# Kernel tuning notes

Measured on AMD Instinct MI355X. Metric: run time of the kernel, lower is better.

The kernel has to match this reference:

```python
import jax, jax.numpy as jnp
import numpy as np

E = 131072   # total messages
N = 8192     # dim_size (num nodes)
D = 256      # input_dim == hidden_dim (forced by h + m add)


def setup_inputs() -> dict:
    key = jax.random.key(0)
    k1, k2, k3, k4, k5 = jax.random.split(key, 5)
    msg = jax.random.normal(k1, (E, D), dtype=jnp.float32)
    index = jax.random.randint(k2, (E,), 0, N)
    t = jax.random.uniform(k3, (E,), dtype=jnp.float32)
    # torch.nn.Linear(D, D) params (kaiming-uniform-ish scale)
    W = jax.random.normal(k4, (D, D), dtype=jnp.float32) / np.sqrt(D)
    b = (jax.random.normal(k5, (D,), dtype=jnp.float32) * 0.01)
    return {"msg": msg, "index": index, "t": t, "dim_size": N, "W": W, "b": b}


def reference(msg, index, t, dim_size, W, b):
    # Original: for each node, sort its messages by t, then run the linear
    # recurrence h <- W @ (m + h) + b starting from h = 0; nodes with no
    # messages keep h = 0. Vectorized: one global stable sort by (index, t),
    # then a single segmented lax.scan with reset at segment boundaries.
    num_msgs, d = msg.shape
    order = jnp.lexsort((t, index))          # primary key: index, secondary: t
    m_sorted = msg[order]                     # [E, d]
    seg = index[order]                        # [E]

    def step(carry, inp):
        h, prev = carry
        m, s = inp
        h_in = jnp.where(s == prev, h, jnp.zeros_like(h))  # reset at new segment
        h_new = (m + h_in) @ W.T + b
        return (h_new, s), h_new

    init = (jnp.zeros((d,), msg.dtype), jnp.asarray(-1, seg.dtype))
    _, ys = jax.lax.scan(step, init, (m_sorted, seg))      # ys: [E, d]

    # final hidden per node = h at the last message of its segment
    pos = jnp.arange(num_msgs)
    last = jax.ops.segment_max(pos, seg, num_segments=dim_size)
    counts = jax.ops.segment_sum(jnp.ones((num_msgs,), jnp.int32), seg,
                                 num_segments=dim_size)
    gathered = ys[jnp.clip(last, 0, num_msgs - 1)]          # [N, d]
    hidden = jnp.where((counts > 0)[:, None], gathered, jnp.zeros_like(gathered))
    return hidden
```

## Files before the change

### kernel.cpp

```cpp
#include <hip/hip_runtime.h>
#include <hip/hip_bf16.h>

#define E_MSGS 131072
#define N_NODES 8192
#define D_DIM 256
#define XA_STRIDE 264

typedef __bf16 bf16x8 __attribute__((ext_vector_type(8)));
typedef float f32x4 __attribute__((ext_vector_type(4)));

#define BAR() asm volatile("s_waitcnt lgkmcnt(0)\n\ts_barrier" ::: "memory")


__global__ void k_count(const int* __restrict__ index, int* __restrict__ counts) {
    int e = blockIdx.x * blockDim.x + threadIdx.x;
    if (e < E_MSGS) atomicAdd(&counts[index[e]], 1);
}

__global__ void k_scan(const int* __restrict__ counts, int* __restrict__ offsets,
                       int* __restrict__ cursors) {
    __shared__ int wsum[16], wpre[16];
    int tid = threadIdx.x, lane = tid & 63, wave = tid >> 6;
    int base = tid * 8;
    int4 c0 = *(const int4*)(counts + base);
    int4 c1 = *(const int4*)(counts + base + 4);
    int v[8] = {c0.x, c0.y, c0.z, c0.w, c1.x, c1.y, c1.z, c1.w};
    int loc[8], sum = 0;
#pragma unroll
    for (int i = 0; i < 8; i++) { loc[i] = sum; sum += v[i]; }
    int incl = sum;
#pragma unroll
    for (int d = 1; d < 64; d <<= 1) {
        int u = __shfl_up(incl, d);
        if (lane >= d) incl += u;
    }
    if (lane == 63) wsum[wave] = incl;
    __syncthreads();
    if (tid < 16) {
        int w = wsum[tid], p = w;
#pragma unroll
        for (int d = 1; d < 16; d <<= 1) {
            int u = __shfl_up(p, d);
            if (tid >= d) p += u;
        }
        wpre[tid] = p - w;
    }
    __syncthreads();
    int ebase = wpre[wave] + incl - sum;
#pragma unroll
    for (int i = 0; i < 8; i++) offsets[base + i] = ebase + loc[i];
    int4 z = {0, 0, 0, 0};
    *(int4*)(cursors + base) = z;
    *(int4*)(cursors + base + 4) = z;
    if (tid == 0) offsets[N_NODES] = E_MSGS;
}

__global__ void k_scatter(const int* __restrict__ index, const int* __restrict__ offsets,
                          int* __restrict__ cursors, int* __restrict__ bucket) {
    int e = blockIdx.x * blockDim.x + threadIdx.x;
    if (e < E_MSGS) {
        int n = index[e];
        int p = offsets[n] + atomicAdd(&cursors[n], 1);
        bucket[p] = e;
    }
}


#define GRU_STEP(SS, CUR, NXT)                                                 \
    {                                                                          \
        _Pragma("unroll") for (int r = 0; r < 4; r++) {                        \
            const float* mrow = msg + (long)sidR[r] * D_DIM;                   \
            _Pragma("unroll") for (int t4 = 0; t4 < 4; t4++)                   \
                NXT[r][t4] = mrow[64 * wave + 16 * t4 + l];                     \
        }                                                                      \
        {                                                                      \
            int row = (SS) + 3 < 64 ? (SS) + 3 : 63;                           \
            int4 sr = *(const int4*)&sid[row][4 * q];                          \
            sidR[0] = sr.x; sidR[1] = sr.y; sidR[2] = sr.z; sidR[3] = sr.w;    \
        }                                                                      \
        const __bf16* buf = xA[(SS) & 1];                                      \
        f32x4 acc[4];                                                          \
        _Pragma("unroll") for (int t4 = 0; t4 < 4; t4++)                       \
            acc[t4] = (f32x4){0.f, 0.f, 0.f, 0.f};                             \
        _Pragma("unroll") for (int c = 0; c < 8; c++) {                        \
            bf16x8 a = *(const bf16x8*)(buf + l * XA_STRIDE + 32 * c + 8 * q); \
            _Pragma("unroll") for (int t4 = 0; t4 < 4; t4++)                   \
                acc[t4] = __builtin_amdgcn_mfma_f32_16x16x32_bf16(             \
                    a, wf[c][t4], acc[t4], 0, 0, 0);                           \
        }                                                                      \
        __bf16* nbuf = xA[((SS) + 1) & 1];                                     \
        _Pragma("unroll") for (int t4 = 0; t4 < 4; t4++) {                     \
            _Pragma("unroll") for (int r = 0; r < 4; r++) {                    \
                float hn = acc[t4][r] + bias[t4];                              \
                bool valid = (SS) < cnt4[r];                                   \
                h[t4][r] = valid ? hn : h[t4][r];                              \
                nbuf[(4 * q + r) * XA_STRIDE + 64 * wave + 16 * t4 + l] =      \
                    (__bf16)(h[t4][r] + CUR[r][t4]);                           \
            }                                                                  \
        }                                                                      \
        BAR();                                                                 \
    }

__launch_bounds__(256, 2)
__global__ void k_gru(const float* __restrict__ msg, const float* __restrict__ t,
                      const int* __restrict__ bucket, const float* __restrict__ W,
                      const float* __restrict__ b, const int* __restrict__ offsets,
                      float* __restrict__ out) {
    __shared__ __bf16 xA[2][16 * XA_STRIDE];
    __shared__ int sid[64][16];

    int tid = threadIdx.x;
    int wave = tid >> 6, lane = tid & 63, q = lane >> 4, l = lane & 15;
    int node0 = blockIdx.x * 16;

    bf16x8 wf[8][4];
#pragma unroll
    for (int t4 = 0; t4 < 4; t4++) {
        const float* wr = W + (64 * wave + 16 * t4 + l) * D_DIM;
#pragma unroll
        for (int c = 0; c < 8; c++) {
            int k0 = 32 * c + 8 * q;
            float4 w0 = *(const float4*)(wr + k0);
            float4 w1 = *(const float4*)(wr + k0 + 4);
            bf16x8 f;
            f[0] = (__bf16)w0.x; f[1] = (__bf16)w0.y; f[2] = (__bf16)w0.z; f[3] = (__bf16)w0.w;
            f[4] = (__bf16)w1.x; f[5] = (__bf16)w1.y; f[6] = (__bf16)w1.z; f[7] = (__bf16)w1.w;
            wf[c][t4] = f;
        }
    }
    float bias[4];
#pragma unroll
    for (int t4 = 0; t4 < 4; t4++) bias[t4] = b[64 * wave + 16 * t4 + l];

    int off4[4], cnt4[4];
#pragma unroll
    for (int r = 0; r < 4; r++) {
        off4[r] = offsets[node0 + 4 * q + r];
        cnt4[r] = offsets[node0 + 4 * q + r + 1] - off4[r];
    }
    int mc = max(max(cnt4[0], cnt4[1]), max(cnt4[2], cnt4[3]));
    mc = max(mc, __shfl_xor(mc, 16));
    mc = max(mc, __shfl_xor(mc, 32));
    int S = mc;

    for (int i = 0; i < 4; i++) {
        int j = 4 * wave + i;
        int beg = offsets[node0 + j];
        int cnt = min(offsets[node0 + j + 1] - beg, 64);
        sid[lane][j] = 0;
        int e = 0; float tv = 0.f;
        if (lane < cnt) { e = bucket[beg + lane]; tv = t[e]; }
        int rank = 0;
        for (int j2 = 0; j2 < cnt; j2++) {
            float tj = __shfl(tv, j2);
            int ej = __shfl(e, j2);
            rank += (tj < tv) || (tj == tv && ej < e);
        }
        if (lane < cnt) sid[rank][j] = e;
    }
    BAR();

    float h[4][4];
#pragma unroll
    for (int t4 = 0; t4 < 4; t4++)
#pragma unroll
        for (int r = 0; r < 4; r++) h[t4][r] = 0.f;

    float mvA[4][4], mvB[4][4];
    int sidR[4];
    int4 sr0 = *(const int4*)&sid[0][4 * q];
    int4 sr1 = *(const int4*)&sid[1][4 * q];
    int4 sr2 = *(const int4*)&sid[2][4 * q];
    int s0[4] = {sr0.x, sr0.y, sr0.z, sr0.w};
    int s1[4] = {sr1.x, sr1.y, sr1.z, sr1.w};
    sidR[0] = sr2.x; sidR[1] = sr2.y; sidR[2] = sr2.z; sidR[3] = sr2.w;
#pragma unroll
    for (int r = 0; r < 4; r++) {
        const float* m0 = msg + (long)s0[r] * D_DIM;
        const float* m1 = msg + (long)s1[r] * D_DIM;
#pragma unroll
        for (int t4 = 0; t4 < 4; t4++) {
            int col = 64 * wave + 16 * t4 + l;
            xA[0][(4 * q + r) * XA_STRIDE + col] = (__bf16)m0[col];
            mvA[r][t4] = m1[col];
        }
    }
    BAR();

    int s = 0;
    while (s < S) {
        GRU_STEP(s, mvA, mvB); s++;
        if (s >= S) break;
        GRU_STEP(s, mvB, mvA); s++;
    }

#pragma unroll
    for (int t4 = 0; t4 < 4; t4++)
#pragma unroll
        for (int r = 0; r < 4; r++)
            out[(long)(node0 + 4 * q + r) * D_DIM + 64 * wave + 16 * t4 + l] = h[t4][r];
}


extern "C" void kernel_launch(void* const* d_in, const int* in_sizes, int n_in,
                              void* d_out, int out_size, void* d_ws, size_t ws_size,
                              hipStream_t stream) {
    const float* msg   = (const float*)d_in[0];
    const int*   index = (const int*)d_in[1];
    const float* t     = (const float*)d_in[2];
    const float* W     = (const float*)d_in[4];
    const float* b     = (const float*)d_in[5];
    float* out = (float*)d_out;

    int* ws = (int*)d_ws;
    int* counts  = ws;
    int* cursors = ws + 8192;
    int* offsets = ws + 16384;
    int* bucket  = ws + 24584;

    hipMemsetAsync(counts, 0, 8192 * sizeof(int), stream);

    k_count<<<E_MSGS / 256, 256, 0, stream>>>(index, counts);
    k_scan<<<1, 1024, 0, stream>>>(counts, offsets, cursors);
    k_scatter<<<E_MSGS / 256, 256, 0, stream>>>(index, offsets, cursors, bucket);
    k_gru<<<N_NODES / 16, 256, 0, stream>>>(msg, t, bucket, W, b, offsets, out);
}
```

Measured before the change: 266.3 us.

## Bucket messages into fixed 64-slot padded arrays and sort nodes by count

Replaces the count/scan/scatter CSR build with a single atomic scatter into fixed 64-slot per-node buckets, which drops one kernel and the prefix scan. A new single-block kernel counting-sorts nodes by message count, descending. Each GRU block then processes 16 nodes of similar length, so fewer recurrence steps are wasted on padding. It also raises wave priority around the MFMA loop. The cost is a hard cap of 64 messages per node, which silently drops the rest, and scattered output writes.

```diff
diff --git a/kernel.cpp b/kernel.cpp
--- a/kernel.cpp
+++ b/kernel.cpp
@@ -12,56 +12,37 @@
 #define BAR() asm volatile("s_waitcnt lgkmcnt(0)\n\ts_barrier" ::: "memory")
 
 
-__global__ void k_count(const int* __restrict__ index, int* __restrict__ counts) {
+__global__ void k_scatter(const int* __restrict__ index, int* __restrict__ cursors,
+                          int* __restrict__ pad) {
     int e = blockIdx.x * blockDim.x + threadIdx.x;
-    if (e < E_MSGS) atomicAdd(&counts[index[e]], 1);
-}
-
-__global__ void k_scan(const int* __restrict__ counts, int* __restrict__ offsets,
-                       int* __restrict__ cursors) {
-    __shared__ int wsum[16], wpre[16];
-    int tid = threadIdx.x, lane = tid & 63, wave = tid >> 6;
-    int base = tid * 8;
-    int4 c0 = *(const int4*)(counts + base);
-    int4 c1 = *(const int4*)(counts + base + 4);
-    int v[8] = {c0.x, c0.y, c0.z, c0.w, c1.x, c1.y, c1.z, c1.w};
-    int loc[8], sum = 0;
-#pragma unroll
-    for (int i = 0; i < 8; i++) { loc[i] = sum; sum += v[i]; }
-    int incl = sum;
-#pragma unroll
-    for (int d = 1; d < 64; d <<= 1) {
-        int u = __shfl_up(incl, d);
-        if (lane >= d) incl += u;
-    }
-    if (lane == 63) wsum[wave] = incl;
+    int n = index[e];
+    int p = atomicAdd(&cursors[n], 1);
+    if (p < 64) pad[(n << 6) + p] = e;
+}
+
+__global__ void k_perm(const int* __restrict__ counts, int* __restrict__ perm) {
+    __shared__ int hist[65];
+    __shared__ int hcur[65];
+    int tid = threadIdx.x;
+    if (tid < 65) hist[tid] = 0;
     __syncthreads();
-    if (tid < 16) {
-        int w = wsum[tid], p = w;
-#pragma unroll
-        for (int d = 1; d < 16; d <<= 1) {
-            int u = __shfl_up(p, d);
-            if (tid >= d) p += u;
-        }
-        wpre[tid] = p - w;
+    int myc[32];
+#pragma unroll
+    for (int i = 0; i < 32; i++) {
+        int c = min(counts[tid * 32 + i], 64);
+        myc[i] = c;
+        atomicAdd(&hist[c], 1);
     }
     __syncthreads();
-    int ebase = wpre[wave] + incl - sum;
-#pragma unroll
-    for (int i = 0; i < 8; i++) offsets[base + i] = ebase + loc[i];
-    int4 z = {0, 0, 0, 0};
-    *(int4*)(cursors + base) = z;
-    *(int4*)(cursors + base + 4) = z;
-    if (tid == 0) offsets[N_NODES] = E_MSGS;
-}
-
-__global__ void k_scatter(const int* __restrict__ index, const int* __restrict__ offsets,
-                          int* __restrict__ cursors, int* __restrict__ bucket) {
-    int e = blockIdx.x * blockDim.x + threadIdx.x;
-    if (e < E_MSGS) {
-        int n = index[e];
-        int p = offsets[n] + atomicAdd(&cursors[n], 1);
-        bucket[p] = e;
+    if (tid == 0) {
+        int run = 0;
+        for (int c = 64; c >= 0; c--) { hcur[c] = run; run += hist[c]; }
+    }
+    __syncthreads();
+#pragma unroll
+    for (int i = 0; i < 32; i++) {
+        int pos = atomicAdd(&hcur[myc[i]], 1);
+        perm[pos] = tid * 32 + i;
     }
 }
 
@@ -82,12 +63,14 @@
         f32x4 acc[4];                                                          \
         _Pragma("unroll") for (int t4 = 0; t4 < 4; t4++)                       \
             acc[t4] = (f32x4){0.f, 0.f, 0.f, 0.f};                             \
+        __builtin_amdgcn_s_setprio(1);                                         \
         _Pragma("unroll") for (int c = 0; c < 8; c++) {                        \
             bf16x8 a = *(const bf16x8*)(buf + l * XA_STRIDE + 32 * c + 8 * q); \
             _Pragma("unroll") for (int t4 = 0; t4 < 4; t4++)                   \
                 acc[t4] = __builtin_amdgcn_mfma_f32_16x16x32_bf16(             \
                     a, wf[c][t4], acc[t4], 0, 0, 0);                           \
         }                                                                      \
+        __builtin_amdgcn_s_setprio(0);                                         \
         __bf16* nbuf = xA[((SS) + 1) & 1];                                     \
         _Pragma("unroll") for (int t4 = 0; t4 < 4; t4++) {                     \
             _Pragma("unroll") for (int r = 0; r < 4; r++) {                    \
@@ -103,9 +86,9 @@
 
 __launch_bounds__(256, 2)
 __global__ void k_gru(const float* __restrict__ msg, const float* __restrict__ t,
-                      const int* __restrict__ bucket, const float* __restrict__ W,
-                      const float* __restrict__ b, const int* __restrict__ offsets,
-                      float* __restrict__ out) {
+                      const int* __restrict__ pad, const float* __restrict__ W,
+                      const float* __restrict__ b, const int* __restrict__ counts,
+                      const int* __restrict__ perm, float* __restrict__ out) {
     __shared__ __bf16 xA[2][16 * XA_STRIDE];
     __shared__ int sid[64][16];
 
@@ -132,24 +115,22 @@
 #pragma unroll
     for (int t4 = 0; t4 < 4; t4++) bias[t4] = b[64 * wave + 16 * t4 + l];
 
-    int off4[4], cnt4[4];
+    int nodeC[4], cnt4[4];
 #pragma unroll
     for (int r = 0; r < 4; r++) {
-        off4[r] = offsets[node0 + 4 * q + r];
-        cnt4[r] = offsets[node0 + 4 * q + r + 1] - off4[r];
-    }
-    int mc = max(max(cnt4[0], cnt4[1]), max(cnt4[2], cnt4[3]));
-    mc = max(mc, __shfl_xor(mc, 16));
-    mc = max(mc, __shfl_xor(mc, 32));
-    int S = mc;
+        int n = perm[node0 + 4 * q + r];
+        nodeC[r] = n;
+        cnt4[r] = min(counts[n], 64);
+    }
+    int S = min(counts[perm[node0]], 64);
 
     for (int i = 0; i < 4; i++) {
         int j = 4 * wave + i;
-        int beg = offsets[node0 + j];
-        int cnt = min(offsets[node0 + j + 1] - beg, 64);
+        int n = perm[node0 + j];
+        int cnt = min(counts[n], 64);
         sid[lane][j] = 0;
         int e = 0; float tv = 0.f;
-        if (lane < cnt) { e = bucket[beg + lane]; tv = t[e]; }
+        if (lane < cnt) { e = pad[(n << 6) + lane]; tv = t[e]; }
         int rank = 0;
         for (int j2 = 0; j2 < cnt; j2++) {
             float tj = __shfl(tv, j2);
@@ -198,7 +179,7 @@
     for (int t4 = 0; t4 < 4; t4++)
 #pragma unroll
         for (int r = 0; r < 4; r++)
-            out[(long)(node0 + 4 * q + r) * D_DIM + 64 * wave + 16 * t4 + l] = h[t4][r];
+            out[(long)nodeC[r] * D_DIM + 64 * wave + 16 * t4 + l] = h[t4][r];
 }
 
 
@@ -213,15 +194,13 @@
     float* out = (float*)d_out;
 
     int* ws = (int*)d_ws;
-    int* counts  = ws;
-    int* cursors = ws + 8192;
-    int* offsets = ws + 16384;
-    int* bucket  = ws + 24584;
-
-    hipMemsetAsync(counts, 0, 8192 * sizeof(int), stream);
-
-    k_count<<<E_MSGS / 256, 256, 0, stream>>>(index, counts);
-    k_scan<<<1, 1024, 0, stream>>>(counts, offsets, cursors);
-    k_scatter<<<E_MSGS / 256, 256, 0, stream>>>(index, offsets, cursors, bucket);
-    k_gru<<<N_NODES / 16, 256, 0, stream>>>(msg, t, bucket, W, b, offsets, out);
-}
+    int* cursors = ws;
+    int* perm    = ws + 8192;
+    int* pad     = ws + 16384;
+
+    hipMemsetAsync(cursors, 0, 8192 * sizeof(int), stream);
+
+    k_scatter<<<E_MSGS / 256, 256, 0, stream>>>(index, cursors, pad);
+    k_perm<<<1, 256, 0, stream>>>(cursors, perm);
+    k_gru<<<N_NODES / 16, 256, 0, stream>>>(msg, t, pad, W, b, cursors, perm, out);
+}
```

Result: no change. 263.5 us (-1.1%).
